# Kernel optimization log

Hardware: AMD Instinct MI355X
Metric: run time of the kernel (lower is better)

The kernel has to match this reference:

```python
import jax, jax.numpy as jnp
import numpy as np

NT = 100000   # total word nodes (B graphs * N nodes)
B = 50        # number of graphs in the batch
E = 1600000   # total edges
V = 15000     # vocab (num_word)
D_IN = 128    # h_inp
D_H = 128     # h_dim


def setup_inputs() -> dict:
    key = jax.random.key(0)
    ks = jax.random.split(key, 12)
    return {
        "node_ids": jax.random.randint(ks[0], (NT,), 0, V),
        "src": jax.random.randint(ks[1], (E,), 0, NT),
        "dst": jax.random.randint(ks[2], (E,), 0, NT),
        "edge_weight": jax.random.uniform(ks[3], (E,), dtype=jnp.float32),
        "y_data": jax.random.uniform(ks[4], (B,), dtype=jnp.float32),
        "word_embeds": jax.random.normal(ks[5], (V, D_IN), dtype=jnp.float32) * 0.1,
        "W1": jax.random.normal(ks[6], (D_IN, D_H), dtype=jnp.float32) * 0.05,
        "b1": jax.random.normal(ks[7], (D_H,), dtype=jnp.float32) * 0.05,
        "W2": jax.random.normal(ks[8], (D_H, D_H), dtype=jnp.float32) * 0.05,
        "b2": jax.random.normal(ks[9], (D_H,), dtype=jnp.float32) * 0.05,
        "W_out": jax.random.normal(ks[10], (D_H, 1), dtype=jnp.float32) * 0.05,
        "b_out": jax.random.normal(ks[11], (1,), dtype=jnp.float32) * 0.05,
    }


def _word_graph_layer(h, W, b, src, dst, edge_weight, deg):
    # Linear projection, then DGL u_mul_e + mean aggregation over incoming edges.
    Wh = h @ W + b                                   # [NT, D]
    m = Wh[src] * edge_weight[:, None]               # gather + edge-weight mul, [E, D]
    s = jax.ops.segment_sum(m, dst, num_segments=NT)  # scatter-add, [NT, D]
    # mean over incoming messages; nodes with no in-edges keep 0 (DGL semantics)
    return jnp.where(deg[:, None] > 0, s / jnp.maximum(deg, 1.0)[:, None], 0.0)


def reference(node_ids, src, dst, edge_weight, y_data, word_embeds,
              W1, b1, W2, b2, W_out, b_out):
    deg = jax.ops.segment_sum(jnp.ones_like(edge_weight), dst, num_segments=NT)
    h = word_embeds[node_ids]                        # [NT, D_IN]
    h = _word_graph_layer(h, W1, b1, src, dst, edge_weight, deg)
    h = jax.nn.leaky_relu(h, negative_slope=0.01)
    h = _word_graph_layer(h, W2, b2, src, dst, edge_weight, deg)
    # per-graph mean pool; equal graph sizes so padded mean == true mean
    word_pool = h.reshape(B, NT // B, D_H).mean(axis=1)   # [B, D_H]
    logits = (word_pool @ W_out + b_out).reshape(-1)      # [B]
    # binary_cross_entropy_with_logits, mean reduction (numerically stable)
    loss = jnp.mean(jnp.maximum(logits, 0.0) - logits * y_data
                    + jnp.log1p(jnp.exp(-jnp.abs(logits))))
    y_pred = jax.nn.sigmoid(logits)[:, None]              # [B, 1]
    return (loss, y_pred)
```

## Files before the change

### kernel.cpp

```cpp
#include <hip/hip_runtime.h>
#include <hip/hip_fp16.h>
#include <math.h>

#define NT 100000
#define B_GRAPHS 50
#define NE 1600000
#define V 15000
#define D 128
#define NODES_PER_GRAPH (NT / B_GRAPHS)

#define POOL_N (B_GRAPHS * D + B_GRAPHS)

#define BSH 8
#define BIN_DSTS 256
#define NBIN ((NT + BIN_DSTS - 1) / BIN_DSTS)
#define SLACK (3 * BIN_DSTS)
#define EPB 4096
#define NFB ((NE + EPB - 1) / EPB)
#define BUF_SORT 5632
#define STAGE_STRIDE 4608
#define PAY_STRIDE (STAGE_STRIDE + SLACK)
#define PAY_TAIL 512
#define PR 16
#define PROJ_BLOCKS ((V + PR - 1) / PR)

#define SS_STRIDE 4608
#define NPART NBIN

typedef _Float16 half2_t __attribute__((ext_vector_type(2)));

#if defined(__has_builtin)
#if __has_builtin(__builtin_amdgcn_fdot2)
#define HAVE_FDOT2 1
#endif
#endif

__device__ __forceinline__ float dot2acc(unsigned a, unsigned b, float c) {
#ifdef HAVE_FDOT2
  return __builtin_amdgcn_fdot2(__builtin_bit_cast(half2_t, a),
                                __builtin_bit_cast(half2_t, b), c, false);
#else
  float a0 = __half2float(__ushort_as_half((unsigned short)(a & 0xffffu)));
  float a1 = __half2float(__ushort_as_half((unsigned short)(a >> 16)));
  float b0 = __half2float(__ushort_as_half((unsigned short)(b & 0xffffu)));
  float b1 = __half2float(__ushort_as_half((unsigned short)(b >> 16)));
  return fmaf(a1, b1, fmaf(a0, b0, c));
#endif
}

__device__ __forceinline__ unsigned enc2_e5m2(float a, float b) {
  unsigned ha = __half_as_ushort(__float2half(a));
  unsigned hb = __half_as_ushort(__float2half(b));
  ha = ((ha + 0x7fu + ((ha >> 8) & 1u)) >> 8) & 0xffu;
  hb = ((hb + 0x7fu + ((hb >> 8) & 1u)) >> 8) & 0xffu;
  return ha | (hb << 8);
}
__device__ __forceinline__ unsigned enc4_e5m2(float a, float b, float c, float d) {
  return enc2_e5m2(a, b) | (enc2_e5m2(c, d) << 16);
}

__global__ __launch_bounds__(512)
void k_pb(const float* __restrict__ embeds, const float* __restrict__ W1,
          const float* __restrict__ b1, unsigned* __restrict__ P1p8,
          float* __restrict__ pool, int2* __restrict__ payTail,
          const int* __restrict__ src, const int* __restrict__ dst,
          const float* __restrict__ ew, const int* __restrict__ node_ids,
          int* __restrict__ binCursor, int2* __restrict__ stage,
          unsigned* __restrict__ h1p8) {
  __shared__ union {
    struct {
      int h[512], sc[512], gbase[512], cur[512];
      int wsum[8], woff[8];
      unsigned short binOf[EPB];
      int2 buf[EPB];
    } f;
    struct {
      float sE[PR][D];
      float sO[PR][D];
    } p;
  } U;
  int t = threadIdx.x;
  if (blockIdx.x < NFB) {
    int lane = t & 63, wv = t >> 6;
    U.f.h[t] = 0;
    __syncthreads();
    int base = blockIdx.x * EPB;
    int d_[EPB / 512], b_[EPB / 512];
#pragma unroll
    for (int i = 0; i < EPB / 512; ++i) {
      int e = base + i * 512 + t;
      int d = (e < NE) ? dst[e] : -1;
      d_[i] = d;
      b_[i] = (d >= 0) ? (d >> BSH) : -1;
      if (d >= 0) atomicAdd(&U.f.h[b_[i]], 1);
    }
    __syncthreads();
    int c = U.f.h[t];
    int v = c;
#pragma unroll
    for (int off = 1; off < 64; off <<= 1) {
      int x = __shfl_up(v, off);
      if (lane >= off) v += x;
    }
    if (lane == 63) U.f.wsum[wv] = v;
    __syncthreads();
    if (t == 0) {
      int a = 0;
#pragma unroll
      for (int i = 0; i < 8; ++i) { U.f.woff[i] = a; a += U.f.wsum[i]; }
    }
    __syncthreads();
    int incl = v + U.f.woff[wv];
    U.f.sc[t] = incl;
    U.f.cur[t] = incl - c;
    if (t < NBIN && c > 0) U.f.gbase[t] = atomicAdd(&binCursor[t], c);
    __syncthreads();
    int total = U.f.sc[511];
#pragma unroll
    for (int i = 0; i < EPB / 512; ++i) {
      int e = base + i * 512 + t;
      if (e < NE) {
        int s = src[e];
        unsigned uw = __float_as_uint(ew[e]);
        unsigned wb = (uw + 0x7fffu + ((uw >> 16) & 1u)) & 0xffff0000u;
        int wid = node_ids[s];
        int dl = d_[i] & (BIN_DSTS - 1);
        int p = atomicAdd(&U.f.cur[b_[i]], 1);
        U.f.buf[p] = make_int2((int)(wb | (unsigned)wid), s | (dl << 17));
        U.f.binOf[p] = (unsigned short)b_[i];
      }
    }
    __syncthreads();
    for (int i = t; i < total; i += 512) {
      int b = U.f.binOf[i];
      int local = i - (U.f.sc[b] - U.f.h[b]);
      stage[(size_t)b * STAGE_STRIDE + U.f.gbase[b] + local] = U.f.buf[i];
    }
  } else {
    int pb = blockIdx.x - NFB;
    if (pb == 0) {
      for (int i = t; i < POOL_N; i += 512) pool[i] = 0.f;
      for (int i = t; i < PAY_TAIL; i += 512) payTail[i] = make_int2(0, 0);
      for (int i = t; i < 256 * 32; i += 512) h1p8[(size_t)NT * 32 + i] = 0u;
    }
    int row0 = pb * PR;
    for (int i = t; i < PR * D; i += 512) {
      int r = i >> 7, c = i & 127;
      int vv = row0 + r;
      U.p.sE[r][c] = (vv < V) ? embeds[(size_t)vv * D + c] : 0.f;
    }
    __syncthreads();
    int c = t & 127, rg = (t >> 7) * 4;
    float bd = b1[c];
    float acc[4];
#pragma unroll
    for (int r = 0; r < 4; ++r) acc[r] = bd;
#pragma unroll 4
    for (int k = 0; k < D; ++k) {
      float w = W1[k * D + c];
#pragma unroll
      for (int r = 0; r < 4; ++r) acc[r] = fmaf(U.p.sE[rg + r][k], w, acc[r]);
    }
#pragma unroll
    for (int r = 0; r < 4; ++r) U.p.sO[rg + r][c] = acc[r];
    __syncthreads();
    {
      int r = t >> 5, li = t & 31;
      int vv = row0 + r;
      if (vv < V)
        P1p8[(size_t)vv * 32 + li] =
            enc4_e5m2(U.p.sO[r][4 * li], U.p.sO[r][4 * li + 1],
                      U.p.sO[r][4 * li + 2], U.p.sO[r][4 * li + 3]);
    }
  }
}

__global__ __launch_bounds__(512)
void k_binsort(const int2* __restrict__ stage, const int* __restrict__ binCnt,
               int* __restrict__ rowD, int* __restrict__ cntD,
               int2* __restrict__ pay, float* __restrict__ invDegG,
               float* __restrict__ poolC) {
  __shared__ int h2[BIN_DSTS], cur2[BIN_DSTS];
  __shared__ float invD[BIN_DSTS];
  __shared__ int wsum4[4], woff4[4];
  __shared__ int sh_end;
  __shared__ int2 buf[BUF_SORT];
  int b = blockIdx.x, t = threadIdx.x;
  int lane = t & 63, wv = t >> 6;
  int cnt = binCnt[b];
  int sb = b * STAGE_STRIDE;
  int pb = b * PAY_STRIDE;
  int dst0 = b << BSH;
  int g0 = dst0 / NODES_PER_GRAPH;
  int bnd = (g0 + 1) * NODES_PER_GRAPH - dst0;
  int gg1 = g0 + 1; if (gg1 > B_GRAPHS - 1) gg1 = B_GRAPHS - 1;
  float sg0 = 0.f, sg1 = 0.f;
  if (t < BIN_DSTS) h2[t] = 0;
  __syncthreads();
  for (int i = t; i < cnt; i += 512)
    atomicAdd(&h2[(stage[sb + i].y >> 17) & 255], 1);
  __syncthreads();
  int c = (t < BIN_DSTS) ? h2[t] : 0;
  int pc = (c + 3) & ~3;
  int v = (t < BIN_DSTS) ? pc : 0;
#pragma unroll
  for (int off = 1; off < 64; off <<= 1) {
    int x = __shfl_up(v, off);
    if (lane >= off) v += x;
  }
  if (lane == 63 && wv < 4) wsum4[wv] = v;
  __syncthreads();
  if (t == 0) {
    int a = 0;
#pragma unroll
    for (int i = 0; i < 4; ++i) { woff4[i] = a; a += wsum4[i]; }
    sh_end = a;
  }
  __syncthreads();
  if (t < BIN_DSTS) {
    int myoff = v + woff4[wv] - pc;
    invD[t] = (c > 0) ? (1.0f / (float)c) : 0.0f;
    cur2[t] = myoff;
    int n = dst0 + t;
    if (n < NT) { rowD[n] = pb + myoff; cntD[n] = c; invDegG[n] = invD[t]; }
  }
  __syncthreads();
  int end = sh_end + 24;
  if (end > PAY_STRIDE) end = PAY_STRIDE;
  for (int i = t; i < end; i += 512) buf[i] = make_int2(0, 0);
  __syncthreads();
  for (int i = t; i < cnt; i += 512) {
    int2 r = stage[sb + i];
    int dl = (r.y >> 17) & 255;
    float w = __uint_as_float((unsigned)r.x & 0xffff0000u);
    float wp = w * invD[dl];
    unsigned wh = (unsigned)__half_as_ushort(__float2half(wp));
    int p = atomicAdd(&cur2[dl], 1);
    buf[p] = make_int2((int)((wh << 16) | ((unsigned)r.x & 0xffffu)), r.y & 0x1ffff);
    if (dl >= bnd) sg1 += wp; else sg0 += wp;
  }
  __syncthreads();
  for (int i = t; i < end; i += 512) pay[pb + i] = buf[i];
#pragma unroll
  for (int off = 32; off > 0; off >>= 1) {
    sg0 += __shfl_down(sg0, off);
    sg1 += __shfl_down(sg1, off);
  }
  if (lane == 0) {
    if (sg0 != 0.f) atomicAdd(&poolC[g0], sg0);
    if (sg1 != 0.f) atomicAdd(&poolC[gg1], sg1);
  }
}

__global__ __launch_bounds__(512)
void k_sfill(const int* __restrict__ src, const int* __restrict__ dst,
             const float* __restrict__ ew, const float* __restrict__ invDegG,
             int* __restrict__ sCursor, unsigned* __restrict__ stageS) {
  __shared__ struct {
    int h[512], sc[512], gbase[512], cur[512];
    int wsum[8], woff[8];
    unsigned short binOf[EPB];
    unsigned buf[EPB];
  } S;
  int t = threadIdx.x, lane = t & 63, wv = t >> 6;
  S.h[t] = 0;
  __syncthreads();
  int base = blockIdx.x * EPB;
  int s_[EPB / 512], b_[EPB / 512];
#pragma unroll
  for (int i = 0; i < EPB / 512; ++i) {
    int e = base + i * 512 + t;
    int s = (e < NE) ? src[e] : -1;
    s_[i] = s;
    b_[i] = (s >= 0) ? (s >> 8) : -1;
    if (s >= 0) atomicAdd(&S.h[b_[i]], 1);
  }
  __syncthreads();
  int c = S.h[t];
  int v = c;
#pragma unroll
  for (int off = 1; off < 64; off <<= 1) {
    int x = __shfl_up(v, off);
    if (lane >= off) v += x;
  }
  if (lane == 63) S.wsum[wv] = v;
  __syncthreads();
  if (t == 0) {
    int a = 0;
#pragma unroll
    for (int i = 0; i < 8; ++i) { S.woff[i] = a; a += S.wsum[i]; }
  }
  __syncthreads();
  int incl = v + S.woff[wv];
  S.sc[t] = incl;
  S.cur[t] = incl - c;
  if (t < NBIN && c > 0) S.gbase[t] = atomicAdd(&sCursor[t], c);
  __syncthreads();
  int total = S.sc[511];
#pragma unroll
  for (int i = 0; i < EPB / 512; ++i) {
    int e = base + i * 512 + t;
    if (e < NE) {
      int d = dst[e];
      float wp = ew[e] * invDegG[d];
      unsigned wh = (unsigned)__half_as_ushort(__float2half(wp));
      unsigned g = (unsigned)d / (unsigned)NODES_PER_GRAPH;
      int sl = s_[i] & 255;
      int p = atomicAdd(&S.cur[b_[i]], 1);
      S.buf[p] = (wh << 16) | ((unsigned)sl << 8) | g;
      S.binOf[p] = (unsigned short)b_[i];
    }
  }
  __syncthreads();
  for (int i = t; i < total; i += 512) {
    int b = S.binOf[i];
    int local = i - (S.sc[b] - S.h[b]);
    stageS[(size_t)b * SS_STRIDE + S.gbase[b] + local] = S.buf[i];
  }
}

template<bool USE_WID>
__device__ __forceinline__ int pick_idx(const int4& q, int half) {
  int lo = USE_WID ? (q.x & 0xffff) : q.y;
  int hi = USE_WID ? (q.z & 0xffff) : q.w;
  return half ? hi : lo;
}
__device__ __forceinline__ void consume2h(const int4& q, unsigned v, int half,
                                          __half2& A01, __half2& A23, __half2& SW) {
  unsigned wm = (unsigned)(half ? q.z : q.x);
  unsigned wd = (wm >> 16) | (wm & 0xffff0000u);
  unsigned hp0 = ((v & 0xffu) << 8) | ((v & 0xff00u) << 16);
  unsigned hp1 = ((v >> 8) & 0xff00u) | (v & 0xff000000u);
  __half2 w2 = *(__half2*)&wd;
  A01 = __hfma2(w2, *(__half2*)&hp0, A01);
  A23 = __hfma2(w2, *(__half2*)&hp1, A23);
  SW = __hadd2(SW, w2);
}

template<bool USE_WID>
__device__ __forceinline__ void gather_row(const int2* __restrict__ pay,
                                           const unsigned* __restrict__ tab,
                                           int beg, int cnt, int li, int half,
                                           __half2& A01, __half2& A23, __half2& SW) {
  int G = (cnt + 3) >> 2;
  const int4* __restrict__ pp = (const int4*)(pay + beg);
  int4 q0a = pp[0], q0b = pp[1];
  int4 q1a = pp[2], q1b = pp[3];
  int4 q2a = pp[4], q2b = pp[5];
  int4 q3a = pp[6], q3b = pp[7];
  int4 q4a = pp[8], q4b = pp[9];
  unsigned va0 = tab[(size_t)pick_idx<USE_WID>(q0a, half) * 32 + li];
  unsigned vb0 = tab[(size_t)pick_idx<USE_WID>(q0b, half) * 32 + li];
  unsigned va1 = tab[(size_t)pick_idx<USE_WID>(q1a, half) * 32 + li];
  unsigned vb1 = tab[(size_t)pick_idx<USE_WID>(q1b, half) * 32 + li];
  unsigned va2 = tab[(size_t)pick_idx<USE_WID>(q2a, half) * 32 + li];
  unsigned vb2 = tab[(size_t)pick_idx<USE_WID>(q2b, half) * 32 + li];
  for (int g = 0; g < G; ++g) {
    unsigned vn0 = tab[(size_t)pick_idx<USE_WID>(q3a, half) * 32 + li];
    unsigned vn1 = tab[(size_t)pick_idx<USE_WID>(q3b, half) * 32 + li];
    int4 qna = pp[2 * g + 10];
    int4 qnb = pp[2 * g + 11];
    consume2h(q0a, va0, half, A01, A23, SW);
    consume2h(q0b, vb0, half, A01, A23, SW);
    q0a = q1a; q0b = q1b; q1a = q2a; q1b = q2b; q2a = q3a; q2b = q3b;
    q3a = q4a; q3b = q4b; q4a = qna; q4b = qnb;
    va0 = va1; vb0 = vb1; va1 = va2; vb1 = vb2; va2 = vn0; vb2 = vn1;
  }
}

#define NPW1 10
__global__ void k_agg1(const int2* __restrict__ pay,
                       const int* __restrict__ rowD, const int* __restrict__ cntD,
                       const unsigned* __restrict__ P1p8,
                       unsigned* __restrict__ h1p8) {
  int w = threadIdx.x >> 6, lane = threadIdx.x & 63;
  int li = lane & 31, half = lane >> 5;
  int nbase = blockIdx.x * (4 * NPW1) + w * NPW1;
  for (int i = 0; i < NPW1; ++i) {
    int n = nbase + i;
    int beg = __builtin_amdgcn_readfirstlane(rowD[n]);
    int cnt = __builtin_amdgcn_readfirstlane(cntD[n]);
    __half2 A01 = __half2half2(__float2half(0.f));
    __half2 A23 = A01, SW = A01;
    gather_row<true>(pay, P1p8, beg, cnt, li, half, A01, A23, SW);
    float2 f01 = __half22float2(A01);
    float2 f23 = __half22float2(A23);
    float a0 = f01.x, a1 = f01.y, a2 = f23.x, a3 = f23.y;
    a0 += __shfl_down(a0, 32);
    a1 += __shfl_down(a1, 32);
    a2 += __shfl_down(a2, 32);
    a3 += __shfl_down(a3, 32);
    if (lane < 32) {
      float x0 = a0, x1 = a1, x2 = a2, x3 = a3;
      x0 = (x0 > 0.f) ? x0 : 0.01f * x0;
      x1 = (x1 > 0.f) ? x1 : 0.01f * x1;
      x2 = (x2 > 0.f) ? x2 : 0.01f * x2;
      x3 = (x3 > 0.f) ? x3 : 0.01f * x3;
      h1p8[(size_t)n * 32 + li] = enc4_e5m2(x0, x1, x2, x3);
    }
  }
}

__global__ __launch_bounds__(512)
void k_cpool(const unsigned* __restrict__ stageS, const int* __restrict__ sCnt,
             const unsigned* __restrict__ h1p8, float* __restrict__ part) {
  __shared__ float Cl[256 * B_GRAPHS];
  __shared__ unsigned Cl2[B_GRAPHS * 128];
  int b = blockIdx.x, t = threadIdx.x;
  for (int i = t; i < 256 * B_GRAPHS; i += 512) Cl[i] = 0.f;
  __syncthreads();
  int cnt = sCnt[b];
  const unsigned* __restrict__ sp_ = stageS + (size_t)b * SS_STRIDE;
  for (int i = t; i < cnt; i += 512) {
    unsigned r = sp_[i];
    int g = (int)(r & 63u);
    int sl = (int)((r >> 8) & 255u);
    float wp = __half2float(__ushort_as_half((unsigned short)(r >> 16)));
    atomicAdd(&Cl[sl * B_GRAPHS + g], wp);
  }
  __syncthreads();
  for (int i = t; i < B_GRAPHS * 128; i += 512) {
    int g = i >> 7, sp = i & 127;
    float lo = Cl[(2 * sp) * B_GRAPHS + g];
    float hi = Cl[(2 * sp + 1) * B_GRAPHS + g];
    __half2 h = __floats2half2_rn(lo, hi);
    Cl2[i] = __builtin_bit_cast(unsigned, h);
  }
  __syncthreads();
  int d = t & 127, gq = t >> 7;
  int row0 = b * 256;
  const unsigned* __restrict__ hp = h1p8 + ((size_t)row0 * 32 + (d >> 2));
  int sh = 8 * (d & 3);
  float acc[13];
#pragma unroll
  for (int j = 0; j < 13; ++j) acc[j] = 0.f;
  for (int s4 = 0; s4 < 32; ++s4) {
    unsigned pk[4];
#pragma unroll
    for (int u = 0; u < 4; ++u) {
      unsigned v0 = hp[0], v1 = hp[32];
      hp += 64;
      pk[u] = (((v0 >> sh) & 0xffu) << 8) | (((v1 >> sh) & 0xffu) << 24);
    }
#pragma unroll
    for (int j = 0; j < 13; ++j) {
      int g = gq + 4 * j;
      if (g < B_GRAPHS) {
        uint4 c4 = *(const uint4*)&Cl2[g * 128 + 4 * s4];
        acc[j] = dot2acc(pk[0], c4.x, acc[j]);
        acc[j] = dot2acc(pk[1], c4.y, acc[j]);
        acc[j] = dot2acc(pk[2], c4.z, acc[j]);
        acc[j] = dot2acc(pk[3], c4.w, acc[j]);
      }
    }
  }
  float* __restrict__ pb = part + (size_t)b * (B_GRAPHS * D);
#pragma unroll
  for (int j = 0; j < 13; ++j) {
    int g = gq + 4 * j;
    if (g < B_GRAPHS) pb[g * D + d] = acc[j];
  }
}

__global__ __launch_bounds__(256)
void k_reduce(const float* __restrict__ part, float* __restrict__ pool) {
  __shared__ float red[3][64];
  int t = threadIdx.x;
  int c = blockIdx.x * 64 + (t & 63);
  int q = t >> 6;
  int p0 = (q * NPART) >> 2, p1 = ((q + 1) * NPART) >> 2;
  float s = 0.f;
#pragma unroll 8
  for (int p = p0; p < p1; ++p) s += part[(size_t)p * (B_GRAPHS * D) + c];
  if (q) red[q - 1][t & 63] = s;
  __syncthreads();
  if (!q) pool[c] = s + red[0][t & 63] + red[1][t & 63] + red[2][t & 63];
}

__global__ void k_final(const float* __restrict__ poolS, const float* __restrict__ poolC,
                        const float* __restrict__ W2, const float* __restrict__ b2,
                        const float* __restrict__ W_out, const float* __restrict__ b_out,
                        const float* __restrict__ y, float* __restrict__ out) {
  __shared__ float w2o[D];
  __shared__ float s2oArr[D];
  __shared__ float s2o_sh;
  __shared__ float logits[64];
  int t = threadIdx.x;
  int w = t >> 6, lane = t & 63;
  if (t < D) {
    float acc = 0.f;
    for (int d = 0; d < D; ++d) acc = fmaf(W2[t * D + d], W_out[d], acc);
    w2o[t] = acc;
  } else {
    int j = t - D;
    s2oArr[j] = b2[j] * W_out[j];
  }
  __syncthreads();
  if (t < 64) {
    float v = s2oArr[lane] + s2oArr[64 + lane];
#pragma unroll
    for (int off = 32; off > 0; off >>= 1) v += __shfl_down(v, off);
    if (lane == 0) s2o_sh = v;
  }
  __syncthreads();
  float s2o = s2o_sh;
  float bout = b_out[0];
  const float invN = 1.0f / (float)NODES_PER_GRAPH;
  for (int g = w; g < B_GRAPHS; g += 4) {
    float v = poolS[g * D + lane] * w2o[lane]
            + poolS[g * D + 64 + lane] * w2o[64 + lane];
#pragma unroll
    for (int off = 32; off > 0; off >>= 1) v += __shfl_down(v, off);
    if (lane == 0) {
      float l = v * invN + poolC[g] * invN * s2o + bout;
      logits[g] = l;
      out[1 + g] = 1.0f / (1.0f + expf(-l));
    }
  }
  __syncthreads();
  if (t < 64) {
    float term = 0.f;
    if (lane < B_GRAPHS) {
      float l = logits[lane];
      term = fmaxf(l, 0.f) - l * y[lane] + log1pf(expf(-fabsf(l)));
    }
#pragma unroll
    for (int off = 32; off > 0; off >>= 1) term += __shfl_down(term, off);
    if (lane == 0) out[0] = term / (float)B_GRAPHS;
  }
}

extern "C" void kernel_launch(void* const* d_in, const int* in_sizes, int n_in,
                              void* d_out, int out_size, void* d_ws, size_t ws_size,
                              hipStream_t stream) {
  const int*   node_ids = (const int*)d_in[0];
  const int*   src      = (const int*)d_in[1];
  const int*   dst      = (const int*)d_in[2];
  const float* ew       = (const float*)d_in[3];
  const float* y        = (const float*)d_in[4];
  const float* embeds   = (const float*)d_in[5];
  const float* W1       = (const float*)d_in[6];
  const float* b1       = (const float*)d_in[7];
  const float* W2       = (const float*)d_in[8];
  const float* b2       = (const float*)d_in[9];
  const float* W_out    = (const float*)d_in[10];
  const float* b_out    = (const float*)d_in[11];
  float* out = (float*)d_out;
  (void)in_sizes; (void)n_in; (void)out_size; (void)ws_size;

  char* ws = (char*)d_ws;
  size_t off = 0;
  auto alloc = [&](size_t bytes) {
    size_t r = off;
    off = (off + bytes + 511) & ~(size_t)511;
    return r;
  };
  size_t o_binCur = alloc(1024 * 4);
  size_t o_pool   = alloc((size_t)POOL_N * 4);
  size_t o_rowD   = alloc((size_t)(NT + 1) * 4);
  size_t o_cntD   = alloc((size_t)NT * 4);
  size_t o_invD   = alloc((size_t)NT * 4);
  size_t o_P1p8   = alloc((size_t)V * 32 * 4);
  size_t o_h1p8   = alloc((size_t)(NT + 256) * 32 * 4);
  size_t o_stage  = alloc((size_t)NBIN * STAGE_STRIDE * 8);
  size_t o_pay    = alloc(((size_t)NBIN * PAY_STRIDE + PAY_TAIL) * 8);
  size_t o_stageS = alloc((size_t)NBIN * SS_STRIDE * 4);

  int*      binCursor= (int*)(ws + o_binCur);
  int*      sCursor  = binCursor + 512;
  float*    pool     = (float*)(ws + o_pool);
  int*      rowD     = (int*)(ws + o_rowD);
  int*      cntD     = (int*)(ws + o_cntD);
  float*    invDegG  = (float*)(ws + o_invD);
  unsigned* P1p8     = (unsigned*)(ws + o_P1p8);
  unsigned* h1p8     = (unsigned*)(ws + o_h1p8);
  int2*     stage    = (int2*)(ws + o_stage);
  int2*     pay      = (int2*)(ws + o_pay);
  unsigned* stageS   = (unsigned*)(ws + o_stageS);
  int2*     payTail  = pay + (size_t)NBIN * PAY_STRIDE;
  float*    part     = (float*)(ws + o_stage);

  (void)hipMemsetAsync(binCursor, 0, 1024 * 4, stream);
  k_pb<<<NFB + PROJ_BLOCKS, 512, 0, stream>>>(embeds, W1, b1, P1p8, pool, payTail,
                                              src, dst, ew, node_ids, binCursor, stage,
                                              h1p8);
  k_binsort<<<NBIN, 512, 0, stream>>>(stage, binCursor, rowD, cntD, pay, invDegG,
                                      pool + B_GRAPHS * D);
  k_sfill<<<NFB, 512, 0, stream>>>(src, dst, ew, invDegG, sCursor, stageS);
  k_agg1<<<NT / (4 * NPW1), 256, 0, stream>>>(pay, rowD, cntD, P1p8, h1p8);
  k_cpool<<<NBIN, 512, 0, stream>>>(stageS, sCursor, h1p8, part);
  k_reduce<<<B_GRAPHS * D / 64, 256, 0, stream>>>(part, pool);
  k_final<<<1, 256, 0, stream>>>(pool, pool + B_GRAPHS * D, W2, b2, W_out, b_out, y, out);
}
```

Measured before the change: 293.2 us.

## Fuse source-bin staging into binsort and simplify gather pipeline

Removes the separate k_sfill kernel and builds the source-binned stageS records inside k_binsort, reusing the already-staged edges and the per-bin inverse degree. This drops one launch, a full re-read of src/dst/edge weights and the invDegG global array. The scattered global writes to stageS now go straight from per-edge atomics rather than through an LDS-staged coalesced write. The gather loop also drops its 5-deep prefetch to 1-deep, drops the unused weight-sum accumulator and uses byte-permute instructions for decoding. That cuts registers but may expose more latency.

```diff
diff --git a/kernel.cpp b/kernel.cpp
--- a/kernel.cpp
+++ b/kernel.cpp
@@ -178,10 +178,11 @@
 __global__ __launch_bounds__(512)
 void k_binsort(const int2* __restrict__ stage, const int* __restrict__ binCnt,
                int* __restrict__ rowD, int* __restrict__ cntD,
-               int2* __restrict__ pay, float* __restrict__ invDegG,
-               float* __restrict__ poolC) {
+               int2* __restrict__ pay, int* __restrict__ sCursor,
+               unsigned* __restrict__ stageS, float* __restrict__ poolC) {
   __shared__ int h2[BIN_DSTS], cur2[BIN_DSTS];
   __shared__ float invD[BIN_DSTS];
+  __shared__ int hS[512], curS[512];
   __shared__ int wsum4[4], woff4[4];
   __shared__ int sh_end;
   __shared__ int2 buf[BUF_SORT];
@@ -196,10 +197,15 @@
   int gg1 = g0 + 1; if (gg1 > B_GRAPHS - 1) gg1 = B_GRAPHS - 1;
   float sg0 = 0.f, sg1 = 0.f;
   if (t < BIN_DSTS) h2[t] = 0;
-  __syncthreads();
-  for (int i = t; i < cnt; i += 512)
-    atomicAdd(&h2[(stage[sb + i].y >> 17) & 255], 1);
-  __syncthreads();
+  hS[t] = 0;
+  __syncthreads();
+  for (int i = t; i < cnt; i += 512) {
+    int yv = stage[sb + i].y;
+    atomicAdd(&h2[(yv >> 17) & 255], 1);
+    atomicAdd(&hS[(yv & 0x1ffff) >> 8], 1);
+  }
+  __syncthreads();
+  if (t < NBIN && hS[t] > 0) curS[t] = atomicAdd(&sCursor[t], hS[t]);
   int c = (t < BIN_DSTS) ? h2[t] : 0;
   int pc = (c + 3) & ~3;
   int v = (t < BIN_DSTS) ? pc : 0;
@@ -222,7 +228,7 @@
     invD[t] = (c > 0) ? (1.0f / (float)c) : 0.0f;
     cur2[t] = myoff;
     int n = dst0 + t;
-    if (n < NT) { rowD[n] = pb + myoff; cntD[n] = c; invDegG[n] = invD[t]; }
+    if (n < NT) { rowD[n] = pb + myoff; cntD[n] = c; }
   }
   __syncthreads();
   int end = sh_end + 24;
@@ -232,11 +238,17 @@
   for (int i = t; i < cnt; i += 512) {
     int2 r = stage[sb + i];
     int dl = (r.y >> 17) & 255;
+    int srcn = r.y & 0x1ffff;
     float w = __uint_as_float((unsigned)r.x & 0xffff0000u);
     float wp = w * invD[dl];
     unsigned wh = (unsigned)__half_as_ushort(__float2half(wp));
     int p = atomicAdd(&cur2[dl], 1);
-    buf[p] = make_int2((int)((wh << 16) | ((unsigned)r.x & 0xffffu)), r.y & 0x1ffff);
+    buf[p] = make_int2((int)((wh << 16) | ((unsigned)r.x & 0xffffu)), srcn);
+    int g = (dl >= bnd) ? gg1 : g0;
+    int sbin = srcn >> 8;
+    int pos = atomicAdd(&curS[sbin], 1);
+    stageS[(size_t)sbin * SS_STRIDE + pos] =
+        (wh << 16) | ((unsigned)(srcn & 255) << 8) | (unsigned)g;
     if (dl >= bnd) sg1 += wp; else sg0 += wp;
   }
   __syncthreads();
@@ -252,119 +264,36 @@
   }
 }
 
-__global__ __launch_bounds__(512)
-void k_sfill(const int* __restrict__ src, const int* __restrict__ dst,
-             const float* __restrict__ ew, const float* __restrict__ invDegG,
-             int* __restrict__ sCursor, unsigned* __restrict__ stageS) {
-  __shared__ struct {
-    int h[512], sc[512], gbase[512], cur[512];
-    int wsum[8], woff[8];
-    unsigned short binOf[EPB];
-    unsigned buf[EPB];
-  } S;
-  int t = threadIdx.x, lane = t & 63, wv = t >> 6;
-  S.h[t] = 0;
-  __syncthreads();
-  int base = blockIdx.x * EPB;
-  int s_[EPB / 512], b_[EPB / 512];
-#pragma unroll
-  for (int i = 0; i < EPB / 512; ++i) {
-    int e = base + i * 512 + t;
-    int s = (e < NE) ? src[e] : -1;
-    s_[i] = s;
-    b_[i] = (s >= 0) ? (s >> 8) : -1;
-    if (s >= 0) atomicAdd(&S.h[b_[i]], 1);
-  }
-  __syncthreads();
-  int c = S.h[t];
-  int v = c;
-#pragma unroll
-  for (int off = 1; off < 64; off <<= 1) {
-    int x = __shfl_up(v, off);
-    if (lane >= off) v += x;
-  }
-  if (lane == 63) S.wsum[wv] = v;
-  __syncthreads();
-  if (t == 0) {
-    int a = 0;
-#pragma unroll
-    for (int i = 0; i < 8; ++i) { S.woff[i] = a; a += S.wsum[i]; }
-  }
-  __syncthreads();
-  int incl = v + S.woff[wv];
-  S.sc[t] = incl;
-  S.cur[t] = incl - c;
-  if (t < NBIN && c > 0) S.gbase[t] = atomicAdd(&sCursor[t], c);
-  __syncthreads();
-  int total = S.sc[511];
-#pragma unroll
-  for (int i = 0; i < EPB / 512; ++i) {
-    int e = base + i * 512 + t;
-    if (e < NE) {
-      int d = dst[e];
-      float wp = ew[e] * invDegG[d];
-      unsigned wh = (unsigned)__half_as_ushort(__float2half(wp));
-      unsigned g = (unsigned)d / (unsigned)NODES_PER_GRAPH;
-      int sl = s_[i] & 255;
-      int p = atomicAdd(&S.cur[b_[i]], 1);
-      S.buf[p] = (wh << 16) | ((unsigned)sl << 8) | g;
-      S.binOf[p] = (unsigned short)b_[i];
-    }
-  }
-  __syncthreads();
-  for (int i = t; i < total; i += 512) {
-    int b = S.binOf[i];
-    int local = i - (S.sc[b] - S.h[b]);
-    stageS[(size_t)b * SS_STRIDE + S.gbase[b] + local] = S.buf[i];
-  }
-}
-
-template<bool USE_WID>
-__device__ __forceinline__ int pick_idx(const int4& q, int half) {
-  int lo = USE_WID ? (q.x & 0xffff) : q.y;
-  int hi = USE_WID ? (q.z & 0xffff) : q.w;
-  return half ? hi : lo;
-}
-__device__ __forceinline__ void consume2h(const int4& q, unsigned v, int half,
-                                          __half2& A01, __half2& A23, __half2& SW) {
-  unsigned wm = (unsigned)(half ? q.z : q.x);
-  unsigned wd = (wm >> 16) | (wm & 0xffff0000u);
-  unsigned hp0 = ((v & 0xffu) << 8) | ((v & 0xff00u) << 16);
-  unsigned hp1 = ((v >> 8) & 0xff00u) | (v & 0xff000000u);
-  __half2 w2 = *(__half2*)&wd;
-  A01 = __hfma2(w2, *(__half2*)&hp0, A01);
-  A23 = __hfma2(w2, *(__half2*)&hp1, A23);
-  SW = __hadd2(SW, w2);
-}
-
-template<bool USE_WID>
-__device__ __forceinline__ void gather_row(const int2* __restrict__ pay,
-                                           const unsigned* __restrict__ tab,
-                                           int beg, int cnt, int li, int half,
-                                           __half2& A01, __half2& A23, __half2& SW) {
+__device__ __forceinline__ void consume2p(unsigned s, unsigned v,
+                                          __half2& A01, __half2& A23) {
+  unsigned wd  = __builtin_amdgcn_perm(s, 0u, 0x07060706u);
+  unsigned hp0 = __builtin_amdgcn_perm(v, 0u, 0x05000400u);
+  unsigned hp1 = __builtin_amdgcn_perm(v, 0u, 0x07000600u);
+  __half2 w2 = __builtin_bit_cast(__half2, wd);
+  A01 = __hfma2(w2, __builtin_bit_cast(__half2, hp0), A01);
+  A23 = __hfma2(w2, __builtin_bit_cast(__half2, hp1), A23);
+}
+
+__device__ __forceinline__ void gather_row2(const int2* __restrict__ pay,
+                                            const unsigned* __restrict__ tab,
+                                            int beg, int cnt, int li, int half,
+                                            __half2& A01, __half2& A23) {
   int G = (cnt + 3) >> 2;
   const int4* __restrict__ pp = (const int4*)(pay + beg);
-  int4 q0a = pp[0], q0b = pp[1];
-  int4 q1a = pp[2], q1b = pp[3];
-  int4 q2a = pp[4], q2b = pp[5];
-  int4 q3a = pp[6], q3b = pp[7];
-  int4 q4a = pp[8], q4b = pp[9];
-  unsigned va0 = tab[(size_t)pick_idx<USE_WID>(q0a, half) * 32 + li];
-  unsigned vb0 = tab[(size_t)pick_idx<USE_WID>(q0b, half) * 32 + li];
-  unsigned va1 = tab[(size_t)pick_idx<USE_WID>(q1a, half) * 32 + li];
-  unsigned vb1 = tab[(size_t)pick_idx<USE_WID>(q1b, half) * 32 + li];
-  unsigned va2 = tab[(size_t)pick_idx<USE_WID>(q2a, half) * 32 + li];
-  unsigned vb2 = tab[(size_t)pick_idx<USE_WID>(q2b, half) * 32 + li];
+  int4 qa = pp[0], qb = pp[1];
+  unsigned sa = (unsigned)(half ? qa.z : qa.x);
+  unsigned sb = (unsigned)(half ? qb.z : qb.x);
+  unsigned va = tab[(size_t)(sa & 0xffffu) * 32 + li];
+  unsigned vb = tab[(size_t)(sb & 0xffffu) * 32 + li];
   for (int g = 0; g < G; ++g) {
-    unsigned vn0 = tab[(size_t)pick_idx<USE_WID>(q3a, half) * 32 + li];
-    unsigned vn1 = tab[(size_t)pick_idx<USE_WID>(q3b, half) * 32 + li];
-    int4 qna = pp[2 * g + 10];
-    int4 qnb = pp[2 * g + 11];
-    consume2h(q0a, va0, half, A01, A23, SW);
-    consume2h(q0b, vb0, half, A01, A23, SW);
-    q0a = q1a; q0b = q1b; q1a = q2a; q1b = q2b; q2a = q3a; q2b = q3b;
-    q3a = q4a; q3b = q4b; q4a = qna; q4b = qnb;
-    va0 = va1; vb0 = vb1; va1 = va2; vb1 = vb2; va2 = vn0; vb2 = vn1;
+    int4 na = pp[2 * g + 2], nb = pp[2 * g + 3];
+    unsigned sna = (unsigned)(half ? na.z : na.x);
+    unsigned snb = (unsigned)(half ? nb.z : nb.x);
+    unsigned wa = tab[(size_t)(sna & 0xffffu) * 32 + li];
+    unsigned wb = tab[(size_t)(snb & 0xffffu) * 32 + li];
+    consume2p(sa, va, A01, A23);
+    consume2p(sb, vb, A01, A23);
+    sa = sna; sb = snb; va = wa; vb = wb;
   }
 }
 
@@ -381,8 +310,8 @@
     int beg = __builtin_amdgcn_readfirstlane(rowD[n]);
     int cnt = __builtin_amdgcn_readfirstlane(cntD[n]);
     __half2 A01 = __half2half2(__float2half(0.f));
-    __half2 A23 = A01, SW = A01;
-    gather_row<true>(pay, P1p8, beg, cnt, li, half, A01, A23, SW);
+    __half2 A23 = A01;
+    gather_row2(pay, P1p8, beg, cnt, li, half, A01, A23);
     float2 f01 = __half22float2(A01);
     float2 f23 = __half22float2(A23);
     float a0 = f01.x, a1 = f01.y, a2 = f23.x, a3 = f23.y;
@@ -559,7 +488,6 @@
   size_t o_pool   = alloc((size_t)POOL_N * 4);
   size_t o_rowD   = alloc((size_t)(NT + 1) * 4);
   size_t o_cntD   = alloc((size_t)NT * 4);
-  size_t o_invD   = alloc((size_t)NT * 4);
   size_t o_P1p8   = alloc((size_t)V * 32 * 4);
   size_t o_h1p8   = alloc((size_t)(NT + 256) * 32 * 4);
   size_t o_stage  = alloc((size_t)NBIN * STAGE_STRIDE * 8);
@@ -571,7 +499,6 @@
   float*    pool     = (float*)(ws + o_pool);
   int*      rowD     = (int*)(ws + o_rowD);
   int*      cntD     = (int*)(ws + o_cntD);
-  float*    invDegG  = (float*)(ws + o_invD);
   unsigned* P1p8     = (unsigned*)(ws + o_P1p8);
   unsigned* h1p8     = (unsigned*)(ws + o_h1p8);
   int2*     stage    = (int2*)(ws + o_stage);
@@ -584,9 +511,8 @@
   k_pb<<<NFB + PROJ_BLOCKS, 512, 0, stream>>>(embeds, W1, b1, P1p8, pool, payTail,
                                               src, dst, ew, node_ids, binCursor, stage,
                                               h1p8);
-  k_binsort<<<NBIN, 512, 0, stream>>>(stage, binCursor, rowD, cntD, pay, invDegG,
-                                      pool + B_GRAPHS * D);
-  k_sfill<<<NFB, 512, 0, stream>>>(src, dst, ew, invDegG, sCursor, stageS);
+  k_binsort<<<NBIN, 512, 0, stream>>>(stage, binCursor, rowD, cntD, pay, sCursor,
+                                      stageS, pool + B_GRAPHS * D);
   k_agg1<<<NT / (4 * NPW1), 256, 0, stream>>>(pay, rowD, cntD, P1p8, h1p8);
   k_cpool<<<NBIN, 512, 0, stream>>>(stageS, sCursor, h1p8, part);
   k_reduce<<<B_GRAPHS * D / 64, 256, 0, stream>>>(part, pool);
```

Result: faster. 264.5 us (-9.8%).
